# Kernel tuning notes

Hardware: AMD Instinct MI355X
Metric: run time of the kernel (lower is better)

The kernel has to match this reference:

```python
import jax, jax.numpy as jnp
import numpy as np

B, S, HID = 2, 2048, 2048
H, HKV, HD = 16, 8, 128
INPUT_CHUNK, RET_CHUNK = 256, 64
NUM_CHUNKS = S // INPUT_CHUNK - 1          # 7 retrieval chunks
INPUT_START = NUM_CHUNKS * RET_CHUNK       # 448
KV_LEN = S + INPUT_START                   # 2496
SCALE = HD ** -0.5


def _document_id():
    d = np.zeros(KV_LEN, np.int32)
    d[INPUT_START:] = -1
    for i in range(NUM_CHUNKS):            # retrieval chunks get ids 1..NUM_CHUNKS
        d[RET_CHUNK * i: RET_CHUNK * (i + 1)] = i + 1
    for i in range(1, NUM_CHUNKS + 1):     # input chunk i (i>=1) gets id i
        d[INPUT_START + INPUT_CHUNK * i: INPUT_START + INPUT_CHUNK * (i + 1)] = i
    return d


def _causal_retrieval_mask():
    d = _document_id()
    q = np.arange(S)[:, None]
    kv = np.arange(KV_LEN)[None, :]
    causal = (q + INPUT_START >= kv) & (kv > INPUT_START)
    docm = (d[q + INPUT_START] == d[kv]) & (kv < INPUT_START)
    return jnp.asarray(causal | docm)      # [S, KV_LEN] bool


_MASK = _causal_retrieval_mask()


def rotate_half(x):
    x1, x2 = jnp.split(x, 2, axis=-1)
    return jnp.concatenate([-x2, x1], axis=-1)


def setup_inputs() -> dict:
    key = jax.random.key(0)
    ks = jax.random.split(key, 8)
    hidden_states = jax.random.normal(ks[0], (B, S, HID), jnp.float32)
    # standard llama RoPE tables
    pos = jnp.arange(S, dtype=jnp.float32)
    inv = 1.0 / (10000.0 ** (jnp.arange(0, HD, 2, dtype=jnp.float32) / HD))
    f = pos[:, None] * inv[None, :]
    emb = jnp.concatenate([f, f], axis=-1)
    cos = jnp.broadcast_to(jnp.cos(emb), (B, S, HD)).astype(jnp.float32)
    sin = jnp.broadcast_to(jnp.sin(emb), (B, S, HD)).astype(jnp.float32)
    retrieval_key_states = jax.random.normal(ks[1], (B * NUM_CHUNKS, HKV, RET_CHUNK, HD), jnp.float32)
    retrieval_value_states = jax.random.normal(ks[2], (B * NUM_CHUNKS, HKV, RET_CHUNK, HD), jnp.float32)
    s = 0.02
    Wq = jax.random.normal(ks[3], (HID, H * HD), jnp.float32) * s
    Wk = jax.random.normal(ks[4], (HID, HKV * HD), jnp.float32) * s
    Wv = jax.random.normal(ks[5], (HID, HKV * HD), jnp.float32) * s
    Wo = jax.random.normal(ks[6], (H * HD, HID), jnp.float32) * s
    return {"hidden_states": hidden_states, "cos": cos, "sin": sin,
            "retrieval_key_states": retrieval_key_states,
            "retrieval_value_states": retrieval_value_states,
            "Wq": Wq, "Wk": Wk, "Wv": Wv, "Wo": Wo}


def reference(hidden_states, cos, sin, retrieval_key_states, retrieval_value_states, Wq, Wk, Wv, Wo):
    b = hidden_states.shape[0]
    # QKV projections (bias=False), -> [b, h, s, d]
    q = (hidden_states @ Wq).reshape(b, S, H, HD).transpose(0, 2, 1, 3)
    k = (hidden_states @ Wk).reshape(b, S, HKV, HD).transpose(0, 2, 1, 3)
    v = (hidden_states @ Wv).reshape(b, S, HKV, HD).transpose(0, 2, 1, 3)
    # RoPE (cos/sin unsqueezed over heads)
    c = cos[:, None]
    sn = sin[:, None]
    q = q * c + rotate_half(q) * sn
    k = k * c + rotate_half(k) * sn
    # retrieval KV: (b*nc, hkv, rc, d) -> (b, hkv, nc*rc, d)
    rk = retrieval_key_states.reshape(b, NUM_CHUNKS, HKV, RET_CHUNK, HD).transpose(0, 2, 1, 3, 4).reshape(b, HKV, NUM_CHUNKS * RET_CHUNK, HD)
    rv = retrieval_value_states.reshape(b, NUM_CHUNKS, HKV, RET_CHUNK, HD).transpose(0, 2, 1, 3, 4).reshape(b, HKV, NUM_CHUNKS * RET_CHUNK, HD)
    k_all = jnp.concatenate([rk, k], axis=2)     # [b, hkv, KV_LEN, d]
    v_all = jnp.concatenate([rv, v], axis=2)
    # GQA: repeat kv heads
    g = H // HKV
    k_all = jnp.repeat(k_all, g, axis=1)
    v_all = jnp.repeat(v_all, g, axis=1)
    scores = jnp.einsum('bhqd,bhkd->bhqk', q, k_all) * SCALE
    neg = jnp.finfo(scores.dtype).min
    scores = jnp.where(_MASK[None, None], scores, neg)
    probs = jax.nn.softmax(scores, axis=-1)
    # fully-masked rows (q_idx=0) -> 0 output, matching flex_attention semantics
    probs = jnp.where(_MASK[None, None], probs, 0.0)
    attn = jnp.einsum('bhqk,bhkd->bhqd', probs, v_all)   # [b, H, S, HD]
    # NOTE: source reshapes (b, H, S, HD) directly to (b, S, H*HD) with NO transpose
    attn = attn.reshape(b, S, H * HD)
    return attn @ Wo
```

## Files before the change

kernel.cpp:

```cpp
#include <hip/hip_runtime.h>

#define B_ 2
#define S_ 2048
#define HID_ 2048
#define H_ 16
#define HKV_ 8
#define HD_ 128
#define NCH_ 7
#define RET_ 64
#define IST_ 448
#define KVL_ 2496
#define SCALE_ 0.08838834764831845f
#define SC2_ (0.08838834764831845f * 1.44269504088896340f)
#define MCAP_ 16.0f

typedef __attribute__((ext_vector_type(8))) short short8;
typedef __attribute__((ext_vector_type(4))) float f32x4;

static __device__ __forceinline__ unsigned short f2bf(float f) {
    unsigned u = __float_as_uint(f);
    unsigned r = (u + 0x7fffu + ((u >> 16) & 1u)) >> 16;
    return (unsigned short)r;
}
static __device__ __forceinline__ float bf2f(unsigned short x) {
    return __uint_as_float(((unsigned)x) << 16);
}

#define GLL16(gp, lp) __builtin_amdgcn_global_load_lds( \
    (__attribute__((address_space(1))) void*)(void*)(gp), \
    (__attribute__((address_space(3))) void*)(void*)(lp), 16, 0, 0)

__global__ __launch_bounds__(256) void prep_in_kernel(const float* __restrict__ hidden,
                                                      const float* __restrict__ Wq,
                                                      const float* __restrict__ Wk,
                                                      const float* __restrict__ Wv,
                                                      const float* __restrict__ Wo,
                                                      unsigned short* __restrict__ hb,
                                                      unsigned short* __restrict__ wqkvT,
                                                      unsigned short* __restrict__ woT) {
    const int bid = blockIdx.x;
    const int tid = threadIdx.x;
    if (bid < 8192) {
        int i = bid * 256 + tid;
        float4 v = ((const float4*)hidden)[i];
        ushort4 o;
        o.x = f2bf(v.x); o.y = f2bf(v.y); o.z = f2bf(v.z); o.w = f2bf(v.w);
        ((ushort4*)hb)[i] = o;
    } else {
        __shared__ float t[32][33];
        const int tbid = bid - 8192;
        const int z = tbid >> 12;
        const int xy = tbid & 4095;
        const int k0 = (xy & 63) << 5, n0 = (xy >> 6) << 5;
        const float* W;
        unsigned short* WT;
        int N;
        if (z == 0)      { W = Wq; WT = wqkvT;                        N = 2048; }
        else if (z == 1) { W = Wk; WT = wqkvT + (size_t)2048 * 2048;  N = 1024; }
        else if (z == 2) { W = Wv; WT = wqkvT + (size_t)3072 * 2048;  N = 1024; }
        else             { W = Wo; WT = woT;                          N = 2048; }
        if (n0 >= N) return;
        const int tx = tid & 31, ty = tid >> 5;
#pragma unroll
        for (int i = 0; i < 4; i++)
            t[ty + i * 8][tx] = W[(size_t)(k0 + ty + i * 8) * N + n0 + tx];
        __syncthreads();
#pragma unroll
        for (int i = 0; i < 4; i++)
            WT[(size_t)(n0 + ty + i * 8) * 2048 + k0 + tx] = f2bf(t[tx][ty + i * 8]);
    }
}

template <int BN, typename OT>
__global__ __launch_bounds__(512, 2) void gemm256(const unsigned short* __restrict__ A,
                                                  const unsigned short* __restrict__ BT,
                                                  OT* __restrict__ C,
                                                  int M, int N, int K) {
    constexpr int NJ = BN / 64;
    __shared__ short As[2][16384];
    __shared__ short Bs[2][BN * 64];
    const int tid = threadIdx.x;
    const int wid = tid >> 6, lane = tid & 63;
    const int lq = lane & 15, lk = lane >> 4;
    const int wm = wid >> 2, wn = wid & 3;
    const int bm = blockIdx.x, bn = blockIdx.y;

    const int rowin = tid >> 3;
    const int koff = (((tid & 7) ^ (rowin & 7)) << 3);
    const size_t abase = (size_t)(bm * 256 + rowin) * K;
    const size_t bbase = (size_t)(bn * BN + rowin) * K;
    const int ldst = wid * 512;

    f32x4 acc[8][NJ] = {};

    auto stage = [&](int buf, int k0) {
#pragma unroll
        for (int r = 0; r < 4; r++)
            GLL16(A + abase + (size_t)(r * 64) * K + k0 + koff, &As[buf][r * 4096 + ldst]);
#pragma unroll
        for (int r = 0; r < NJ; r++)
            GLL16(BT + bbase + (size_t)(r * 64) * K + k0 + koff, &Bs[buf][r * 4096 + ldst]);
    };

    const int nk = K >> 6;
    stage(0, 0);
    __syncthreads();
    for (int t = 0; t < nk; t++) {
        const int cur = t & 1;
        if (t + 1 < nk) stage(cur ^ 1, (t + 1) << 6);
        short8 bf[2][NJ];
#pragma unroll
        for (int j = 0; j < NJ; j++)
#pragma unroll
            for (int kk = 0; kk < 2; kk++) {
                const int row = wn * (BN / 4) + j * 16 + lq;
                bf[kk][j] = *(const short8*)&Bs[cur][row * 64 +
                                                     (((kk * 4 + lk) ^ (lq & 7)) << 3)];
            }
#pragma unroll
        for (int p = 0; p < 4; p++) {
            short8 af0[2], af1[2];
#pragma unroll
            for (int kk = 0; kk < 2; kk++) {
                const int r0 = wm * 128 + (2 * p) * 16 + lq;
                const int r1 = wm * 128 + (2 * p + 1) * 16 + lq;
                af0[kk] = *(const short8*)&As[cur][r0 * 64 +
                                                   (((kk * 4 + lk) ^ (lq & 7)) << 3)];
                af1[kk] = *(const short8*)&As[cur][r1 * 64 +
                                                   (((kk * 4 + lk) ^ (lq & 7)) << 3)];
            }
            __builtin_amdgcn_s_setprio(1);
#pragma unroll
            for (int j = 0; j < NJ; j++)
#pragma unroll
                for (int kk = 0; kk < 2; kk++) {
                    acc[2 * p][j] =
                        __builtin_amdgcn_mfma_f32_16x16x32_bf16(bf[kk][j], af0[kk], acc[2 * p][j], 0, 0, 0);
                    acc[2 * p + 1][j] =
                        __builtin_amdgcn_mfma_f32_16x16x32_bf16(bf[kk][j], af1[kk], acc[2 * p + 1][j], 0, 0, 0);
                }
            __builtin_amdgcn_s_setprio(0);
        }
        __syncthreads();
    }
#pragma unroll
    for (int i = 0; i < 8; i++) {
        const size_t row = (size_t)(bm * 256 + wm * 128 + i * 16 + lq);
#pragma unroll
        for (int j = 0; j < NJ; j++) {
            const size_t col = (size_t)(bn * BN + wn * (BN / 4) + j * 16 + lk * 4);
            if constexpr (sizeof(OT) == 2) {
                ushort4 u;
                u.x = f2bf(acc[i][j][0]);
                u.y = f2bf(acc[i][j][1]);
                u.z = f2bf(acc[i][j][2]);
                u.w = f2bf(acc[i][j][3]);
                *(ushort4*)&C[row * N + col] = u;
            } else {
                *(f32x4*)&C[row * N + col] = acc[i][j];
            }
        }
    }
}

__global__ __launch_bounds__(256) void prep_kv_kernel(const unsigned short* __restrict__ qkvraw,
                                                      const float* __restrict__ cosb,
                                                      const float* __restrict__ sinb,
                                                      const float* __restrict__ rk,
                                                      const float* __restrict__ rv,
                                                      unsigned short* __restrict__ kall,
                                                      unsigned short* __restrict__ vt) {
    const int bid = blockIdx.x;
    const int tid = threadIdx.x;
    if (bid < 8192) {
        size_t idx = (size_t)bid * 256 + tid;
        int d = idx & 63;
        int hk = (idx >> 6) & 7;
        size_t bs = idx >> 9;
        size_t base = bs * 4096 + 2048 + hk * 128 + d;
        int b = (int)(bs >> 11), s = (int)(bs & 2047);
        float x1 = bf2f(qkvraw[base]), x2 = bf2f(qkvraw[base + 64]);
        float c1 = cosb[(size_t)s * 128 + d], sn1 = sinb[(size_t)s * 128 + d];
        float c2 = cosb[(size_t)s * 128 + d + 64], sn2 = sinb[(size_t)s * 128 + d + 64];
        size_t o = ((size_t)(b * HKV_ + hk) * KVL_ + IST_ + s) * HD_ + d;
        kall[o] = f2bf(x1 * c1 - x2 * sn1);
        kall[o + 64] = f2bf(x2 * c2 + x1 * sn2);
    } else if (bid < 11776) {
        size_t idx = (size_t)(bid - 8192) * 256 + tid;
        int d = idx & 127;
        int r = (idx >> 7) & 63;
        int hk = (idx >> 13) & 7;
        int bc = (int)(idx >> 16);
        int b = bc / NCH_, ch = bc % NCH_;
        kall[((size_t)(b * HKV_ + hk) * KVL_ + ch * RET_ + r) * HD_ + d] = f2bf(rk[idx]);
    } else {
        const int vbid = bid - 11776;
        const int tx = tid & 31, ty = tid >> 5;
        if (vbid < 4096) {
            __shared__ unsigned short t[32][33];
            const int d0 = (vbid & 3) << 5, s0 = ((vbid >> 2) & 63) << 5;
            const int bh = vbid >> 8;
            const int b = bh >> 3, hk = bh & 7;
#pragma unroll
            for (int i = 0; i < 4; i++)
                t[ty + i * 8][tx] =
                    qkvraw[(size_t)(b * S_ + s0 + ty + i * 8) * 4096 + 3072 + hk * 128 + d0 + tx];
            __syncthreads();
#pragma unroll
            for (int i = 0; i < 4; i++)
                vt[((size_t)(b * HKV_ + hk) * HD_ + d0 + ty + i * 8) * KVL_ + IST_ + s0 + tx] =
                    t[tx][ty + i * 8];
        } else {
            __shared__ float tf[32][33];
            const int bid2 = vbid - 4096;
            const int d0 = (bid2 & 3) << 5;
            const int r0 = ((bid2 >> 2) & 1) << 5;
            const int z = bid2 >> 3;
            const int bc = z >> 3, hk = z & 7;
            const int b = bc / NCH_, ch = bc % NCH_;
#pragma unroll
            for (int i = 0; i < 4; i++)
                tf[ty + i * 8][tx] =
                    rv[((size_t)(bc * HKV_ + hk) * RET_ + r0 + ty + i * 8) * HD_ + d0 + tx];
            __syncthreads();
#pragma unroll
            for (int i = 0; i < 4; i++)
                vt[((size_t)(b * HKV_ + hk) * HD_ + d0 + ty + i * 8) * KVL_ + ch * RET_ + r0 + tx] =
                    f2bf(tf[tx][ty + i * 8]);
        }
    }
}

__global__ __launch_bounds__(1024) void attn_kernel(const unsigned short* __restrict__ qkvraw,
                                                    const unsigned short* __restrict__ kall,
                                                    const unsigned short* __restrict__ vt,
                                                    const float* __restrict__ cosb,
                                                    const float* __restrict__ sinb,
                                                    unsigned short* __restrict__ attnb) {
    __shared__ short Ks[2][16384];
    __shared__ short Vs[2][16384];
    __shared__ short Ps[16][1024];
    const int tid = threadIdx.x;
    const int wid = tid >> 6, lane = tid & 63;
    const int lq = lane & 15, lk = lane >> 4;
    const int pairi = blockIdx.x;
    const int h = blockIdx.y, b = blockIdx.z, hk = h >> 1;
    const unsigned short* kbase = kall + (size_t)(b * HKV_ + hk) * KVL_ * HD_;
    const unsigned short* vbase = vt + (size_t)(b * HKV_ + hk) * HD_ * KVL_;

    int row_[2], xc_[2];
#pragma unroll
    for (int p = 0; p < 2; p++) {
        int o = p * 16384 + tid * 16;
        row_[p] = o >> 8;
        xc_[p] = (tid & 15) ^ (row_[p] & 7);
    }
    short* psw = &Ps[wid][0];

    const int qlo = pairi * 128, qhi = (15 - pairi) * 128;
    const int wgrp = wid >> 3;
    const int qb0 = wgrp ? qhi : qlo;
    const int qbw = qb0 + (wid & 7) * 16;
    const int doc_lo = qlo >> 8;
    const int doc_hi = qhi >> 8;
    const int kvA = RET_ * ((doc_lo >= 1 ? doc_lo : 1) - 1);
    const int kvB = RET_ * (doc_hi - 1);
    const int nt = 17 - pairi;

    const unsigned short* qrp = qkvraw + ((size_t)(b * S_) + qbw + lq) * 4096 + h * 128;
    short8 qr[4];
#pragma unroll
    for (int d = 0; d < 4; d++) qr[d] = *(const short8*)(qrp + d * 32 + lk * 8);
    const float* cosp = cosb + (size_t)(qbw + lq) * 128 + lk * 8;
    const float* sinp = sinb + (size_t)(qbw + lq) * 128 + lk * 8;
    short8 qf[4];
#pragma unroll
    for (int d = 0; d < 4; d++) {
        float4 c0 = *(const float4*)(cosp + d * 32);
        float4 c1 = *(const float4*)(cosp + d * 32 + 4);
        float4 s0 = *(const float4*)(sinp + d * 32);
        float4 s1 = *(const float4*)(sinp + d * 32 + 4);
        const float cc[8] = {c0.x, c0.y, c0.z, c0.w, c1.x, c1.y, c1.z, c1.w};
        const float ss[8] = {s0.x, s0.y, s0.z, s0.w, s1.x, s1.y, s1.z, s1.w};
        const int od = d ^ 2;
        const float sg = (d < 2) ? -1.f : 1.f;
#pragma unroll
        for (int e = 0; e < 8; e++) {
            float x = bf2f((unsigned short)qr[d][e]);
            float y = bf2f((unsigned short)qr[od][e]);
            qf[d][e] = (short)f2bf(fmaf(sg * y, ss[e], x * cc[e]));
        }
    }

    f32x4 o[8] = {};
    float lsump = 0.f;

    auto stage = [&](int buf, int kv0) {
#pragma unroll
        for (int p = 0; p < 2; p++) {
            GLL16(kbase + (size_t)(kv0 + row_[p]) * HD_ + xc_[p] * 8,
                  &Ks[buf][p * 8192 + wid * 512]);
            GLL16(vbase + (size_t)row_[p] * KVL_ + kv0 + xc_[p] * 8,
                  &Vs[buf][p * 8192 + wid * 512]);
        }
    };
    auto stage_ret = [&](int buf) {
#pragma unroll
        for (int p = 0; p < 2; p++) {
            int kr = row_[p];
            int ks = (kr < 64) ? kvA + kr : kvB + (kr - 64);
            GLL16(kbase + (size_t)ks * HD_ + xc_[p] * 8, &Ks[buf][p * 8192 + wid * 512]);
            int vc = (xc_[p] < 8) ? kvA + xc_[p] * 8 : kvB + (xc_[p] - 8) * 8;
            GLL16(vbase + (size_t)row_[p] * KVL_ + vc, &Vs[buf][p * 8192 + wid * 512]);
        }
    };
    auto smpv = [&](f32x4* sa4, int hb8, const char* vb) {
#pragma unroll
        for (int j2 = 0; j2 < 4; j2++) {
            float p0 = __builtin_amdgcn_exp2f(fmaf(sa4[j2][0], SC2_, -MCAP_));
            float p1 = __builtin_amdgcn_exp2f(fmaf(sa4[j2][1], SC2_, -MCAP_));
            float p2 = __builtin_amdgcn_exp2f(fmaf(sa4[j2][2], SC2_, -MCAP_));
            float p3 = __builtin_amdgcn_exp2f(fmaf(sa4[j2][3], SC2_, -MCAP_));
            lsump += (p0 + p1) + (p2 + p3);
            uint2 w;
            asm("v_cvt_pk_bf16_f32 %0, %1, %2" : "=v"(w.x) : "v"(p0), "v"(p1));
            asm("v_cvt_pk_bf16_f32 %0, %1, %2" : "=v"(w.y) : "v"(p2), "v"(p3));
            *(uint2*)((char*)psw + (lq * 128 + ((j2 * 32 + lk * 8) ^ ((lq & 7) << 4)))) = w;
        }
        __builtin_amdgcn_s_setprio(1);
#pragma unroll
        for (int ks = 0; ks < 2; ks++) {
            short8 pa = *(const short8*)((const char*)psw +
                                         (lq * 128 + (((ks * 4 + lk) ^ (lq & 7)) << 4)));
#pragma unroll
            for (int db = 0; db < 8; db++) {
                short8 vf = *(const short8*)(vb + ((db * 16 + lq) * 256 +
                                                   (((hb8 + ks * 4 + lk) ^ (lq & 7)) << 4)));
                o[db] = __builtin_amdgcn_mfma_f32_16x16x32_bf16(pa, vf, o[db], 0, 0, 0);
            }
        }
        __builtin_amdgcn_s_setprio(0);
    };

    stage_ret(0);
    asm volatile("s_waitcnt vmcnt(0)" ::: "memory");
    __syncthreads();
    int cur = 0;
    for (int t = 0; t < nt; t++) {
        if (t + 1 < nt) stage(cur ^ 1, IST_ + t * 128);
        const char* kb = (const char*)&Ks[cur][0];
        const char* vb = (const char*)&Vs[cur][0];
        if (t == 0) {
            const bool retact = (wgrp == 1) || (doc_lo >= 1);
            if (retact) {
                const int hh = wgrp;
                f32x4 sa[4] = {};
                __builtin_amdgcn_s_setprio(1);
#pragma unroll
                for (int d = 0; d < 4; d++)
#pragma unroll
                    for (int j2 = 0; j2 < 4; j2++) {
                        short8 kf = *(const short8*)(kb + (((hh * 4 + j2) * 16 + lq) * 256 +
                                                           (((d * 4 + lk) ^ (lq & 7)) << 4)));
                        sa[j2] = __builtin_amdgcn_mfma_f32_16x16x32_bf16(kf, qf[d], sa[j2], 0, 0, 0);
                    }
                __builtin_amdgcn_s_setprio(0);
                smpv(sa, hh * 8, vb);
            }
        } else {
            const int kv0 = IST_ + (t - 1) * 128;
            const bool active = kv0 <= qbw + 15 + IST_;
            if (active) {
                const bool act2 = (kv0 + 64 <= qbw + 15 + IST_);
                f32x4 sa[8] = {};
                __builtin_amdgcn_s_setprio(1);
#pragma unroll
                for (int d = 0; d < 4; d++)
#pragma unroll
                    for (int j = 0; j < 4; j++) {
                        short8 kf = *(const short8*)(kb + ((j * 16 + lq) * 256 +
                                                           (((d * 4 + lk) ^ (lq & 7)) << 4)));
                        sa[j] = __builtin_amdgcn_mfma_f32_16x16x32_bf16(kf, qf[d], sa[j], 0, 0, 0);
                    }
                if (act2) {
#pragma unroll
                    for (int d = 0; d < 4; d++)
#pragma unroll
                        for (int j = 4; j < 8; j++) {
                            short8 kf = *(const short8*)(kb + ((j * 16 + lq) * 256 +
                                                               (((d * 4 + lk) ^ (lq & 7)) << 4)));
                            sa[j] = __builtin_amdgcn_mfma_f32_16x16x32_bf16(kf, qf[d], sa[j], 0, 0, 0);
                        }
                }
                __builtin_amdgcn_s_setprio(0);
                const int qg = qbw + lq;
                if (kv0 == IST_ || kv0 + 63 > qbw + IST_) {
#pragma unroll
                    for (int j = 0; j < 4; j++)
#pragma unroll
                        for (int r = 0; r < 4; r++) {
                            int kg = kv0 + j * 16 + lk * 4 + r;
                            if (!(kg > IST_ && kg <= qg + IST_)) sa[j][r] = -3e38f;
                        }
                }
                if (act2 && kv0 + 127 > qbw + IST_) {
#pragma unroll
                    for (int j = 4; j < 8; j++)
#pragma unroll
                        for (int r = 0; r < 4; r++) {
                            int kg = kv0 + j * 16 + lk * 4 + r;
                            if (kg > qg + IST_) sa[j][r] = -3e38f;
                        }
                }
                smpv(&sa[0], 0, vb);
                if (act2) smpv(&sa[4], 8, vb);
            }
        }
        if (t + 1 < nt) asm volatile("s_waitcnt vmcnt(0)" ::: "memory");
        __syncthreads();
        cur ^= 1;
    }

    float ls = lsump;
    ls += __shfl_xor(ls, 16);
    ls += __shfl_xor(ls, 32);
    float inv[4];
#pragma unroll
    for (int r = 0; r < 4; r++) {
        float v = __shfl(ls, lk * 4 + r);
        inv[r] = v > 0.f ? 1.f / v : 0.f;
    }
#pragma unroll
    for (int db = 0; db < 8; db++)
#pragma unroll
        for (int r = 0; r < 4; r++) {
            int qg = qbw + lk * 4 + r;
            size_t row = (size_t)b * 2048 + h * 128 + (qg >> 4);
            size_t col = (size_t)(qg & 15) * 128 + db * 16 + lq;
            attnb[row * 2048 + col] = f2bf(o[db][r] * inv[r]);
        }
}

extern "C" void kernel_launch(void* const* d_in, const int* in_sizes, int n_in,
                              void* d_out, int out_size, void* d_ws, size_t ws_size,
                              hipStream_t stream) {
    const float* hidden = (const float*)d_in[0];
    const float* cosb = (const float*)d_in[1];
    const float* sinb = (const float*)d_in[2];
    const float* rk = (const float*)d_in[3];
    const float* rv = (const float*)d_in[4];
    const float* Wq = (const float*)d_in[5];
    const float* Wk = (const float*)d_in[6];
    const float* Wv = (const float*)d_in[7];
    const float* Wo = (const float*)d_in[8];
    float* out = (float*)d_out;

    char* ws = (char*)d_ws;
    unsigned short* hb     = (unsigned short*)(ws + 0);
    unsigned short* wqkvT  = (unsigned short*)(ws + 16777216);
    unsigned short* woT    = (unsigned short*)(ws + 33554432);
    unsigned short* qkvraw = (unsigned short*)(ws + 41943040);
    unsigned short* kallb  = (unsigned short*)(ws + 92274688);
    unsigned short* vtb    = (unsigned short*)(ws + 102498304);
    unsigned short* attnb  = (unsigned short*)(ws + 112721920);

    prep_in_kernel<<<24576, 256, 0, stream>>>(hidden, Wq, Wk, Wv, Wo, hb, wqkvT, woT);

    gemm256<256, unsigned short><<<dim3(16, 16), 512, 0, stream>>>(hb, wqkvT, qkvraw, 4096, 4096, 2048);

    prep_kv_kernel<<<16768, 256, 0, stream>>>(qkvraw, cosb, sinb, rk, rv, kallb, vtb);

    attn_kernel<<<dim3(8, 16, 2), 1024, 0, stream>>>(qkvraw, kallb, vtb, cosb, sinb, attnb);

    gemm256<128, float><<<dim3(16, 16), 512, 0, stream>>>(attnb, woT, out, 4096, 2048, 2048);
}
```

Before: 215.7 us.

## Triple-buffer the output-projection GEMM and vectorize KV preparation

The Wo projection now has its own GEMM kernel with a three-stage LDS ring. It prefetches two K-tiles ahead and waits with explicit vmcnt counts and a bare s_barrier in place of the per-iteration __syncthreads, aiming to hide global-load latency. Separately, the RoPE-on-K and retrieval-K conversion paths in prep_kv now process four elements per thread with vector loads and stores, which cuts the block count. The extra LDS buffer lowers possible occupancy, and the hand-written waitcnt depends on the exact number of issued loads per stage.

```diff
diff --git a/kernel.cpp b/kernel.cpp
--- a/kernel.cpp
+++ b/kernel.cpp
@@ -15,6 +15,7 @@
 #define MCAP_ 16.0f
 
 typedef __attribute__((ext_vector_type(8))) short short8;
+typedef __attribute__((ext_vector_type(4))) short short4v;
 typedef __attribute__((ext_vector_type(4))) float f32x4;
 
 static __device__ __forceinline__ unsigned short f2bf(float f) {
@@ -71,14 +72,13 @@
     }
 }
 
-template <int BN, typename OT>
 __global__ __launch_bounds__(512, 2) void gemm256(const unsigned short* __restrict__ A,
                                                   const unsigned short* __restrict__ BT,
-                                                  OT* __restrict__ C,
+                                                  unsigned short* __restrict__ C,
                                                   int M, int N, int K) {
-    constexpr int NJ = BN / 64;
+    constexpr int NJ = 4;
     __shared__ short As[2][16384];
-    __shared__ short Bs[2][BN * 64];
+    __shared__ short Bs[2][16384];
     const int tid = threadIdx.x;
     const int wid = tid >> 6, lane = tid & 63;
     const int lq = lane & 15, lk = lane >> 4;
@@ -88,7 +88,7 @@
     const int rowin = tid >> 3;
     const int koff = (((tid & 7) ^ (rowin & 7)) << 3);
     const size_t abase = (size_t)(bm * 256 + rowin) * K;
-    const size_t bbase = (size_t)(bn * BN + rowin) * K;
+    const size_t bbase = (size_t)(bn * 256 + rowin) * K;
     const int ldst = wid * 512;
 
     f32x4 acc[8][NJ] = {};
@@ -113,7 +113,7 @@
         for (int j = 0; j < NJ; j++)
 #pragma unroll
             for (int kk = 0; kk < 2; kk++) {
-                const int row = wn * (BN / 4) + j * 16 + lq;
+                const int row = wn * 64 + j * 16 + lq;
                 bf[kk][j] = *(const short8*)&Bs[cur][row * 64 +
                                                      (((kk * 4 + lk) ^ (lq & 7)) << 3)];
             }
@@ -148,17 +148,104 @@
         const size_t row = (size_t)(bm * 256 + wm * 128 + i * 16 + lq);
 #pragma unroll
         for (int j = 0; j < NJ; j++) {
-            const size_t col = (size_t)(bn * BN + wn * (BN / 4) + j * 16 + lk * 4);
-            if constexpr (sizeof(OT) == 2) {
-                ushort4 u;
-                u.x = f2bf(acc[i][j][0]);
-                u.y = f2bf(acc[i][j][1]);
-                u.z = f2bf(acc[i][j][2]);
-                u.w = f2bf(acc[i][j][3]);
-                *(ushort4*)&C[row * N + col] = u;
-            } else {
-                *(f32x4*)&C[row * N + col] = acc[i][j];
-            }
+            const size_t col = (size_t)(bn * 256 + wn * 64 + j * 16 + lk * 4);
+            ushort4 u;
+            u.x = f2bf(acc[i][j][0]);
+            u.y = f2bf(acc[i][j][1]);
+            u.z = f2bf(acc[i][j][2]);
+            u.w = f2bf(acc[i][j][3]);
+            *(ushort4*)&C[row * N + col] = u;
+        }
+    }
+}
+
+__global__ __launch_bounds__(512) void gemm256_wo(const unsigned short* __restrict__ A,
+                                                  const unsigned short* __restrict__ BT,
+                                                  float* __restrict__ C,
+                                                  int M, int N, int K) {
+    __shared__ short As[3][16384];
+    __shared__ short Bs[3][8192];
+    const int tid = threadIdx.x;
+    const int wid = tid >> 6, lane = tid & 63;
+    const int lq = lane & 15, lk = lane >> 4;
+    const int wm = wid >> 2, wn = wid & 3;
+    const int bm = blockIdx.x, bn = blockIdx.y;
+
+    const int rowin = tid >> 3;
+    const int koff = (((tid & 7) ^ (rowin & 7)) << 3);
+    const size_t abase = (size_t)(bm * 256 + rowin) * K;
+    const size_t bbase = (size_t)(bn * 128 + rowin) * K;
+    const int ldst = wid * 512;
+
+    f32x4 acc[8][2] = {};
+
+    auto stage = [&](int slot, int k0) {
+#pragma unroll
+        for (int r = 0; r < 4; r++)
+            GLL16(A + abase + (size_t)(r * 64) * K + k0 + koff, &As[slot][r * 4096 + ldst]);
+#pragma unroll
+        for (int r = 0; r < 2; r++)
+            GLL16(BT + bbase + (size_t)(r * 64) * K + k0 + koff, &Bs[slot][r * 4096 + ldst]);
+    };
+
+    const int nk = K >> 6;
+    stage(0, 0);
+    stage(1, 64);
+    int cs = 0, ss = 2;
+    for (int t = 0; t < nk; t++) {
+        if (t + 1 < nk) {
+            asm volatile("s_waitcnt vmcnt(6)" ::: "memory");
+        } else {
+            asm volatile("s_waitcnt vmcnt(0)" ::: "memory");
+        }
+        __builtin_amdgcn_s_barrier();
+        __builtin_amdgcn_sched_barrier(0);
+        if (t + 2 < nk) {
+            stage(ss, (t + 2) << 6);
+            ss = (ss == 2) ? 0 : ss + 1;
+        }
+        short8 bf[2][2];
+#pragma unroll
+        for (int j = 0; j < 2; j++)
+#pragma unroll
+            for (int kk = 0; kk < 2; kk++) {
+                const int row = wn * 32 + j * 16 + lq;
+                bf[kk][j] = *(const short8*)&Bs[cs][row * 64 +
+                                                    (((kk * 4 + lk) ^ (lq & 7)) << 3)];
+            }
+#pragma unroll
+        for (int p = 0; p < 4; p++) {
+            short8 af0[2], af1[2];
+#pragma unroll
+            for (int kk = 0; kk < 2; kk++) {
+                const int r0 = wm * 128 + (2 * p) * 16 + lq;
+                const int r1 = wm * 128 + (2 * p + 1) * 16 + lq;
+                af0[kk] = *(const short8*)&As[cs][r0 * 64 +
+                                                  (((kk * 4 + lk) ^ (lq & 7)) << 3)];
+                af1[kk] = *(const short8*)&As[cs][r1 * 64 +
+                                                  (((kk * 4 + lk) ^ (lq & 7)) << 3)];
+            }
+            __builtin_amdgcn_s_setprio(1);
+#pragma unroll
+            for (int j = 0; j < 2; j++)
+#pragma unroll
+                for (int kk = 0; kk < 2; kk++) {
+                    acc[2 * p][j] =
+                        __builtin_amdgcn_mfma_f32_16x16x32_bf16(bf[kk][j], af0[kk], acc[2 * p][j], 0, 0, 0);
+                    acc[2 * p + 1][j] =
+                        __builtin_amdgcn_mfma_f32_16x16x32_bf16(bf[kk][j], af1[kk], acc[2 * p + 1][j], 0, 0, 0);
+                }
+            __builtin_amdgcn_s_setprio(0);
+        }
+        cs = (cs == 2) ? 0 : cs + 1;
+    }
+#pragma unroll
+    for (int i = 0; i < 8; i++) {
+        const size_t row = (size_t)(bm * 256 + wm * 128 + i * 16 + lq);
+#pragma unroll
+        for (int j = 0; j < 2; j++) {
+            const size_t col = (size_t)(bn * 128 + wn * 32 + j * 16 + lk * 4);
+            *(f32x4*)&C[row * N + col] = acc[i][j];
         }
     }
 }
@@ -172,29 +259,48 @@
                                                       unsigned short* __restrict__ vt) {
     const int bid = blockIdx.x;
     const int tid = threadIdx.x;
-    if (bid < 8192) {
-        size_t idx = (size_t)bid * 256 + tid;
-        int d = idx & 63;
-        int hk = (idx >> 6) & 7;
-        size_t bs = idx >> 9;
-        size_t base = bs * 4096 + 2048 + hk * 128 + d;
+    if (bid < 2048) {
+        unsigned u = (unsigned)bid * 256 + tid;
+        int d0 = (u & 15) << 2;
+        int hk = (u >> 4) & 7;
+        unsigned bs = u >> 7;
         int b = (int)(bs >> 11), s = (int)(bs & 2047);
-        float x1 = bf2f(qkvraw[base]), x2 = bf2f(qkvraw[base + 64]);
-        float c1 = cosb[(size_t)s * 128 + d], sn1 = sinb[(size_t)s * 128 + d];
-        float c2 = cosb[(size_t)s * 128 + d + 64], sn2 = sinb[(size_t)s * 128 + d + 64];
-        size_t o = ((size_t)(b * HKV_ + hk) * KVL_ + IST_ + s) * HD_ + d;
-        kall[o] = f2bf(x1 * c1 - x2 * sn1);
-        kall[o + 64] = f2bf(x2 * c2 + x1 * sn2);
-    } else if (bid < 11776) {
-        size_t idx = (size_t)(bid - 8192) * 256 + tid;
-        int d = idx & 127;
-        int r = (idx >> 7) & 63;
-        int hk = (idx >> 13) & 7;
-        int bc = (int)(idx >> 16);
+        size_t base = (size_t)bs * 4096 + 2048 + hk * 128 + d0;
+        short4v x1 = *(const short4v*)(qkvraw + base);
+        short4v x2 = *(const short4v*)(qkvraw + base + 64);
+        float4 c1 = *(const float4*)(cosb + (size_t)s * 128 + d0);
+        float4 s1 = *(const float4*)(sinb + (size_t)s * 128 + d0);
+        float4 c2 = *(const float4*)(cosb + (size_t)s * 128 + d0 + 64);
+        float4 s2 = *(const float4*)(sinb + (size_t)s * 128 + d0 + 64);
+        const float cc1[4] = {c1.x, c1.y, c1.z, c1.w}, ss1[4] = {s1.x, s1.y, s1.z, s1.w};
+        const float cc2[4] = {c2.x, c2.y, c2.z, c2.w}, ss2[4] = {s2.x, s2.y, s2.z, s2.w};
+        size_t o = ((size_t)(b * HKV_ + hk) * KVL_ + IST_ + s) * HD_ + d0;
+        ushort4 w1, w2;
+        unsigned short r1[4], r2[4];
+#pragma unroll
+        for (int e = 0; e < 4; e++) {
+            float a = bf2f((unsigned short)x1[e]);
+            float bb = bf2f((unsigned short)x2[e]);
+            r1[e] = f2bf(a * cc1[e] - bb * ss1[e]);
+            r2[e] = f2bf(bb * cc2[e] + a * ss2[e]);
+        }
+        w1.x = r1[0]; w1.y = r1[1]; w1.z = r1[2]; w1.w = r1[3];
+        w2.x = r2[0]; w2.y = r2[1]; w2.z = r2[2]; w2.w = r2[3];
+        *(ushort4*)(kall + o) = w1;
+        *(ushort4*)(kall + o + 64) = w2;
+    } else if (bid < 2944) {
+        unsigned u = (unsigned)(bid - 2048) * 256 + tid;
+        int d0 = (u & 31) << 2;
+        int r = (u >> 5) & 63;
+        int hk = (u >> 11) & 7;
+        int bc = (int)(u >> 14);
         int b = bc / NCH_, ch = bc % NCH_;
-        kall[((size_t)(b * HKV_ + hk) * KVL_ + ch * RET_ + r) * HD_ + d] = f2bf(rk[idx]);
+        float4 v = *(const float4*)(rk + (((size_t)(bc * HKV_ + hk) * RET_ + r) * HD_ + d0));
+        ushort4 w;
+        w.x = f2bf(v.x); w.y = f2bf(v.y); w.z = f2bf(v.z); w.w = f2bf(v.w);
+        *(ushort4*)(kall + ((size_t)(b * HKV_ + hk) * KVL_ + ch * RET_ + r) * HD_ + d0) = w;
     } else {
-        const int vbid = bid - 11776;
+        const int vbid = bid - 2944;
         const int tx = tid & 31, ty = tid >> 5;
         if (vbid < 4096) {
             __shared__ unsigned short t[32][33];
@@ -466,11 +572,11 @@
 
     prep_in_kernel<<<24576, 256, 0, stream>>>(hidden, Wq, Wk, Wv, Wo, hb, wqkvT, woT);
 
-    gemm256<256, unsigned short><<<dim3(16, 16), 512, 0, stream>>>(hb, wqkvT, qkvraw, 4096, 4096, 2048);
-
-    prep_kv_kernel<<<16768, 256, 0, stream>>>(qkvraw, cosb, sinb, rk, rv, kallb, vtb);
+    gemm256<<<dim3(16, 16), 512, 0, stream>>>(hb, wqkvT, qkvraw, 4096, 4096, 2048);
+
+    prep_kv_kernel<<<7936, 256, 0, stream>>>(qkvraw, cosb, sinb, rk, rv, kallb, vtb);
 
     attn_kernel<<<dim3(8, 16, 2), 1024, 0, stream>>>(qkvraw, kallb, vtb, cosb, sinb, attnb);
 
-    gemm256<128, float><<<dim3(16, 16), 512, 0, stream>>>(attnb, woT, out, 4096, 2048, 2048);
-}
+    gemm256_wo<<<dim3(16, 16), 512, 0, stream>>>(attnb, woT, out, 4096, 2048, 2048);
+}
```

New measurement: 223.5 us. +3.6%, slower.
